# Performance work log

Hardware: AMD Instinct MI355X
Metric: run time of the kernel (lower is better)

The kernel has to match this reference:

```python
import math
import jax, jax.numpy as jnp
import numpy as np

B, L, D = 2, 2048, 512
S, P = 4, 16  # n_orthogonal_sets, planes_per_set
TP = S * P


def setup_inputs() -> dict:
    key = jax.random.key(0)
    ks = jax.random.split(key, 12)
    sc = 0.02
    return {
        "x": jax.random.normal(ks[0], (B, L, D), dtype=jnp.float32),
        "set_weights": jnp.ones((S,), dtype=jnp.float32),
        "kw1": jax.random.normal(ks[1], (D, D), dtype=jnp.float32) * sc,
        "kb1": jnp.zeros((D,), dtype=jnp.float32),
        "kw2": jax.random.normal(ks[2], (D, TP), dtype=jnp.float32) * sc,
        "kb2": jnp.zeros((TP,), dtype=jnp.float32),
        "qw1": jax.random.normal(ks[3], (D, D), dtype=jnp.float32) * sc,
        "qb1": jnp.zeros((D,), dtype=jnp.float32),
        "qw2": jax.random.normal(ks[4], (D, TP), dtype=jnp.float32) * sc,
        "qb2": jnp.zeros((TP,), dtype=jnp.float32),
        "vw": jax.random.normal(ks[5], (D, D), dtype=jnp.float32) * sc,
        "vb": jnp.zeros((D,), dtype=jnp.float32),
        "ln_g": jnp.ones((D,), dtype=jnp.float32),
        "ln_b": jnp.zeros((D,), dtype=jnp.float32),
        "ow": jax.random.normal(ks[6], (D, D), dtype=jnp.float32) * sc,
        "ob": jnp.zeros((D,), dtype=jnp.float32),
    }


def reference(x, set_weights, kw1, kb1, kw2, kb2, qw1, qb1, qw2, qb2, vw, vb, ln_g, ln_b, ow, ob):
    b, l, d = x.shape
    # phase encoders: Linear -> GELU(exact) -> Linear, tanh * pi
    kp = jnp.tanh(jax.nn.gelu(x @ kw1 + kb1, approximate=False) @ kw2 + kb2) * math.pi
    qp = jnp.tanh(jax.nn.gelu(x @ qw1 + qb1, approximate=False) @ qw2 + qb2) * math.pi
    kp = kp.reshape(b, l, S, P)
    qp = qp.reshape(b, l, S, P)
    V = x @ vw + vb  # real values; phasor complex handled as (re, im)
    w = jax.nn.softmax(set_weights)
    total = jnp.zeros((b, l, d), dtype=x.dtype)
    for s in range(S):
        kc, ksn = jnp.cos(kp[:, :, s, :]), jnp.sin(kp[:, :, s, :])  # [b,l,P]
        # bound = e^{i kp} * V (V real); memory = cumsum over time
        Mre = jnp.cumsum(kc[..., None] * V[:, :, None, :], axis=1)  # [b,l,P,d]
        Mim = jnp.cumsum(ksn[..., None] * V[:, :, None, :], axis=1)
        # Re(memory * conj(e^{i qp})) summed over planes
        r = (jnp.einsum('blpd,blp->bld', Mre, jnp.cos(qp[:, :, s, :]))
             + jnp.einsum('blpd,blp->bld', Mim, jnp.sin(qp[:, :, s, :])))
        total = total + w[s] * r
    positions = jnp.arange(1, l + 1, dtype=x.dtype)
    norm = jnp.sqrt(positions * P)[None, :, None]
    y = total / norm
    mu = jnp.mean(y, axis=-1, keepdims=True)
    var = jnp.mean((y - mu) ** 2, axis=-1, keepdims=True)
    yn = (y - mu) / jnp.sqrt(var + 1e-5) * ln_g + ln_b
    return x + yn @ ow + ob
```

## Files before the change

### kernel.cpp

```cpp
#include <hip/hip_runtime.h>
#include <math.h>

constexpr int NB = 2;
constexpr int LQ = 2048;
constexpr int DD = 512;
constexpr int PPL = 16;
constexpr int TPP = 64;
constexpr int FF = 128;
constexpr int NC = 32;
constexpr int TC = 64;
constexpr float PI_F = 3.14159265358979323846f;

typedef __attribute__((ext_vector_type(4))) float f32x4;
typedef __attribute__((ext_vector_type(8))) short bf16x8;

static __device__ __forceinline__ unsigned short f2bf(float x) {
    union { float f; unsigned u; } v; v.f = x;
    unsigned r = v.u + 0x7fff + ((v.u >> 16) & 1);
    return (unsigned short)(r >> 16);
}
static __device__ __forceinline__ float bf2f(unsigned short u) {
    union { unsigned u; float f; } v; v.u = ((unsigned)u) << 16;
    return v.f;
}

__global__ __launch_bounds__(256) void prep_kernel(
    const float* __restrict__ kw1, const float* __restrict__ qw1,
    const float* __restrict__ vw, const float* __restrict__ ow,
    const float* __restrict__ kw2, const float* __restrict__ qw2,
    unsigned short* __restrict__ kw1t, unsigned short* __restrict__ qw1t,
    unsigned short* __restrict__ vwt, unsigned short* __restrict__ owt,
    unsigned short* __restrict__ kw2t, unsigned short* __restrict__ qw2t)
{
    __shared__ float t[32][33];
    const int id = blockIdx.x;
    const int tid = threadIdx.x;
    const float* W;
    unsigned short* O;
    int K, N, n0, k0;
    if (id < 1024) {
        const int mat = id >> 8, rem = id & 255;
        W = (mat == 0) ? kw1 : (mat == 1) ? qw1 : (mat == 2) ? vw : ow;
        O = (mat == 0) ? kw1t : (mat == 1) ? qw1t : (mat == 2) ? vwt : owt;
        K = DD; N = DD;
        n0 = (rem & 15) * 32; k0 = (rem >> 4) * 32;
    } else {
        const int rid = id - 1024;
        const int mat = rid >> 5, rem = rid & 31;
        W = mat ? qw2 : kw2;
        O = mat ? qw2t : kw2t;
        K = DD; N = TPP;
        n0 = (rem & 1) * 32; k0 = (rem >> 1) * 32;
    }
    const int tx = tid & 31, ty = tid >> 5;
#pragma unroll
    for (int i = 0; i < 4; ++i)
        t[ty + 8 * i][tx] = W[(size_t)(k0 + ty + 8 * i) * N + n0 + tx];
    __syncthreads();
#pragma unroll
    for (int i = 0; i < 4; ++i)
        O[(size_t)(n0 + ty + 8 * i) * K + k0 + tx] = f2bf(t[tx][ty + 8 * i]);
}

__global__ __launch_bounds__(256) void mgemm_fused(
    const float* __restrict__ X,
    const unsigned short* __restrict__ kw1t, const unsigned short* __restrict__ qw1t,
    const unsigned short* __restrict__ vwt,
    const float* __restrict__ kb1, const float* __restrict__ qb1, const float* __restrict__ vb,
    unsigned short* __restrict__ hkb, unsigned short* __restrict__ hqb,
    unsigned short* __restrict__ Vt)
{
    const int z = blockIdx.z;
    const unsigned short* Bt = (z == 0) ? kw1t : (z == 1) ? qw1t : vwt;
    const float* bias = (z == 0) ? kb1 : (z == 1) ? qb1 : vb;
    unsigned short* obf = (z == 0) ? hkb : (z == 1) ? hqb : Vt;
    const int K = DD, N = DD;

    __shared__ unsigned short As[128 * 72];
    __shared__ unsigned short Bs[128 * 72];
    const int tid = threadIdx.x;
    const int w = tid >> 6, lane = tid & 63, grp = lane >> 4, lid = lane & 15;
    const int wr = w >> 1, wc = w & 1;
    const int row0 = blockIdx.y * 128, col0 = blockIdx.x * 128;
    f32x4 acc[4][4];
#pragma unroll
    for (int m = 0; m < 4; ++m)
#pragma unroll
        for (int n = 0; n < 4; ++n) acc[m][n] = (f32x4)0.f;

    for (int k0 = 0; k0 < K; k0 += 64) {
        float4 a0[4], a1[4];
        bf16x8 vbv[4];
#pragma unroll
        for (int i = 0; i < 4; ++i) {
            const int c = tid + i * 256;
            const float* ap = X + (size_t)(row0 + (c >> 3)) * K + k0 + (c & 7) * 8;
            a0[i] = *(const float4*)ap;
            a1[i] = *(const float4*)(ap + 4);
            vbv[i] = *(const bf16x8*)(Bt + (size_t)(col0 + (c >> 3)) * K + k0 + (c & 7) * 8);
        }
        __syncthreads();
#pragma unroll
        for (int i = 0; i < 4; ++i) {
            const int c = tid + i * 256;
            ushort4 u0 = {f2bf(a0[i].x), f2bf(a0[i].y), f2bf(a0[i].z), f2bf(a0[i].w)};
            ushort4 u1 = {f2bf(a1[i].x), f2bf(a1[i].y), f2bf(a1[i].z), f2bf(a1[i].w)};
            *(ushort4*)(As + (c >> 3) * 72 + (c & 7) * 8) = u0;
            *(ushort4*)(As + (c >> 3) * 72 + (c & 7) * 8 + 4) = u1;
            *(bf16x8*)(Bs + (c >> 3) * 72 + (c & 7) * 8) = vbv[i];
        }
        __syncthreads();
#pragma unroll
        for (int kk = 0; kk < 2; ++kk) {
            bf16x8 af[4], bfr[4];
#pragma unroll
            for (int m = 0; m < 4; ++m)
                af[m] = *(const bf16x8*)(As + (wr * 64 + m * 16 + lid) * 72 + kk * 32 + grp * 8);
#pragma unroll
            for (int n = 0; n < 4; ++n)
                bfr[n] = *(const bf16x8*)(Bs + (wc * 64 + n * 16 + lid) * 72 + kk * 32 + grp * 8);
#pragma unroll
            for (int m = 0; m < 4; ++m)
#pragma unroll
                for (int n = 0; n < 4; ++n)
                    acc[m][n] = __builtin_amdgcn_mfma_f32_16x16x32_bf16(af[m], bfr[n], acc[m][n], 0, 0, 0);
        }
    }
#pragma unroll
    for (int m = 0; m < 4; ++m) {
#pragma unroll
        for (int n = 0; n < 4; ++n) {
            const int col = col0 + wc * 64 + n * 16 + lid;
            const float bc = bias[col];
            if (z == 2) {
                const int rowb = row0 + wr * 64 + m * 16 + grp * 4;
                const int b = rowb >> 11, l = rowb & (LQ - 1);
                const int c = l >> 6, t0 = l & 63;
                ushort4 u;
                u.x = f2bf(acc[m][n][0] + bc);
                u.y = f2bf(acc[m][n][1] + bc);
                u.z = f2bf(acc[m][n][2] + bc);
                u.w = f2bf(acc[m][n][3] + bc);
                *(ushort4*)(Vt + ((size_t)((b * NC + c) * DD) + col) * TC + t0) = u;
            } else {
#pragma unroll
                for (int r = 0; r < 4; ++r) {
                    const int row = row0 + wr * 64 + m * 16 + grp * 4 + r;
                    float v = acc[m][n][r] + bc;
                    v = 0.5f * v * (1.0f + erff(v * 0.70710678118654752f));
                    obf[(size_t)row * N + col] = f2bf(v);
                }
            }
        }
    }
}

__global__ __launch_bounds__(256) void phase_fused(
    const unsigned short* __restrict__ hkb, const unsigned short* __restrict__ hqb,
    const unsigned short* __restrict__ kw2t, const unsigned short* __restrict__ qw2t,
    const float* __restrict__ kb2, const float* __restrict__ qb2,
    const float* __restrict__ sw,
    unsigned short* __restrict__ CKb, unsigned short* __restrict__ CQb,
    unsigned short* __restrict__ CKt)
{
    const int isq = blockIdx.y;
    const unsigned short* A = isq ? hqb : hkb;
    const unsigned short* Bt = isq ? qw2t : kw2t;
    const float* b2 = isq ? qb2 : kb2;
    unsigned short* FROW = isq ? CQb : CKb;
    const int K = DD;

    __shared__ unsigned short As[64 * 72];
    __shared__ unsigned short Bs[64 * 72];
    const int tid = threadIdx.x;
    const int w = tid >> 6, lane = tid & 63, grp = lane >> 4, lid = lane & 15;
    const int row0 = blockIdx.x * 64;
    f32x4 acc[4];
#pragma unroll
    for (int n = 0; n < 4; ++n) acc[n] = (f32x4)0.f;

    for (int k0 = 0; k0 < K; k0 += 64) {
        bf16x8 va[2], vbv[2];
#pragma unroll
        for (int i = 0; i < 2; ++i) {
            const int c = tid + i * 256;
            va[i] = *(const bf16x8*)(A + (size_t)(row0 + (c >> 3)) * K + k0 + (c & 7) * 8);
            vbv[i] = *(const bf16x8*)(Bt + (size_t)(c >> 3) * K + k0 + (c & 7) * 8);
        }
        __syncthreads();
#pragma unroll
        for (int i = 0; i < 2; ++i) {
            const int c = tid + i * 256;
            *(bf16x8*)(As + (c >> 3) * 72 + (c & 7) * 8) = va[i];
            *(bf16x8*)(Bs + (c >> 3) * 72 + (c & 7) * 8) = vbv[i];
        }
        __syncthreads();
#pragma unroll
        for (int kk = 0; kk < 2; ++kk) {
            bf16x8 af, bfr[4];
            af = *(const bf16x8*)(As + (w * 16 + lid) * 72 + kk * 32 + grp * 8);
#pragma unroll
            for (int n = 0; n < 4; ++n)
                bfr[n] = *(const bf16x8*)(Bs + (n * 16 + lid) * 72 + kk * 32 + grp * 8);
#pragma unroll
            for (int n = 0; n < 4; ++n)
                acc[n] = __builtin_amdgcn_mfma_f32_16x16x32_bf16(af, bfr[n], acc[n], 0, 0, 0);
        }
    }
    float wsm[4] = {1.f, 1.f, 1.f, 1.f};
    if (isq) {
        float s0 = sw[0], s1 = sw[1], s2 = sw[2], s3 = sw[3];
        float mx = fmaxf(fmaxf(s0, s1), fmaxf(s2, s3));
        float e0 = __expf(s0 - mx), e1 = __expf(s1 - mx), e2 = __expf(s2 - mx), e3 = __expf(s3 - mx);
        float inv = 1.0f / (e0 + e1 + e2 + e3);
        wsm[0] = e0 * inv; wsm[1] = e1 * inv; wsm[2] = e2 * inv; wsm[3] = e3 * inv;
    }
#pragma unroll
    for (int n = 0; n < 4; ++n) {
        const int p = n * 16 + lid;
        const float bc = b2[p];
        const float wg = isq ? wsm[p >> 4] : 1.0f;
#pragma unroll
        for (int r = 0; r < 4; ++r) {
            const int row = row0 + w * 16 + grp * 4 + r;
            float u = acc[n][r] + bc;
            float th = 1.0f - 2.0f / (__expf(2.0f * u) + 1.0f);
            float ph = th * PI_F;
            float sp, cp;
            __sincosf(ph, &sp, &cp);
            const unsigned short cb = f2bf(cp * wg), sb = f2bf(sp * wg);
            FROW[(size_t)row * FF + 2 * p + 0] = cb;
            FROW[(size_t)row * FF + 2 * p + 1] = sb;
            if (!isq) {
                const int b = row >> 11, l = row & (LQ - 1);
                const int c = l >> 6, t = l & 63;
                const size_t base = ((size_t)(b * NC + c) * FF) * TC;
                CKt[base + (size_t)(2 * p + 0) * TC + t] = cb;
                CKt[base + (size_t)(2 * p + 1) * TC + t] = sb;
            }
        }
    }
}

__global__ __launch_bounds__(256) void passA_mfma(
    const unsigned short* __restrict__ Vt, const unsigned short* __restrict__ CKt,
    unsigned short* __restrict__ Stp)
{
    const int tid = threadIdx.x;
    const int w = tid >> 6, lane = tid & 63, grp = lane >> 4, lid = lane & 15;
    const int dq = blockIdx.x, c = blockIdx.y, b = blockIdx.z;
    const int d0 = dq * 128 + w * 32;
    const size_t cb = (size_t)(b * NC + c);
    f32x4 acc[2][8];
#pragma unroll
    for (int md = 0; md < 2; ++md)
#pragma unroll
        for (int nf = 0; nf < 8; ++nf) acc[md][nf] = (f32x4)0.f;
#pragma unroll
    for (int kt = 0; kt < 2; ++kt) {
        bf16x8 av[2], bk[8];
#pragma unroll
        for (int md = 0; md < 2; ++md)
            av[md] = *(const bf16x8*)(Vt + (cb * DD + d0 + md * 16 + lid) * TC + kt * 32 + grp * 8);
#pragma unroll
        for (int nf = 0; nf < 8; ++nf)
            bk[nf] = *(const bf16x8*)(CKt + (cb * FF + nf * 16 + lid) * TC + kt * 32 + grp * 8);
#pragma unroll
        for (int md = 0; md < 2; ++md)
#pragma unroll
            for (int nf = 0; nf < 8; ++nf)
                acc[md][nf] = __builtin_amdgcn_mfma_f32_16x16x32_bf16(av[md], bk[nf], acc[md][nf], 0, 0, 0);
    }
#pragma unroll
    for (int md = 0; md < 2; ++md)
#pragma unroll
        for (int nf = 0; nf < 8; ++nf)
#pragma unroll
            for (int r = 0; r < 4; ++r) {
                const int d = d0 + md * 16 + grp * 4 + r;
                const int f = nf * 16 + lid;
                Stp[(cb * DD + d) * FF + f] = f2bf(acc[md][nf][r]);
            }
}

__global__ __launch_bounds__(256) void prefix_mfma(
    const unsigned short* __restrict__ Stp, unsigned short* __restrict__ Stb)
{
    const int gid = blockIdx.x * 256 + threadIdx.x;
    const int b = gid >> 16;
    const int df = gid & 65535;
    float run = 0.f;
#pragma unroll
    for (int c = 0; c < NC; ++c) {
        const size_t idx = ((size_t)(b * NC + c) << 16) + df;
        Stb[idx] = f2bf(run);
        run += bf2f(Stp[idx]);
    }
}

__global__ __launch_bounds__(256) void passC_mfma(
    const unsigned short* __restrict__ CQb, const unsigned short* __restrict__ CKb,
    const unsigned short* __restrict__ Vt, const unsigned short* __restrict__ Stb,
    float* __restrict__ R)
{
    __shared__ unsigned short P[64][72];
    const int tid = threadIdx.x;
    const int w = tid >> 6, lane = tid & 63, grp = lane >> 4, lid = lane & 15;
    const int dh = blockIdx.x, c = blockIdx.y, b = blockIdx.z;
    const size_t rowbase = (size_t)b * LQ + c * 64;
    const size_t cb = (size_t)(b * NC + c);
    f32x4 qk[4];
#pragma unroll
    for (int nt = 0; nt < 4; ++nt) qk[nt] = (f32x4)0.f;
#pragma unroll
    for (int kf = 0; kf < 4; ++kf) {
        bf16x8 aq = *(const bf16x8*)(CQb + (rowbase + w * 16 + lid) * FF + kf * 32 + grp * 8);
        bf16x8 bk[4];
#pragma unroll
        for (int nt = 0; nt < 4; ++nt)
            bk[nt] = *(const bf16x8*)(CKb + (rowbase + nt * 16 + lid) * FF + kf * 32 + grp * 8);
#pragma unroll
        for (int nt = 0; nt < 4; ++nt)
            qk[nt] = __builtin_amdgcn_mfma_f32_16x16x32_bf16(aq, bk[nt], qk[nt], 0, 0, 0);
    }
#pragma unroll
    for (int nt = 0; nt < 4; ++nt)
#pragma unroll
        for (int r = 0; r < 4; ++r) {
            const int row = w * 16 + grp * 4 + r;
            const int col = nt * 16 + lid;
            P[row][col] = f2bf(col <= row ? qk[nt][r] : 0.f);
        }
    __syncthreads();
    const int d0 = dh * 128 + w * 32;
    f32x4 racc[4][2];
#pragma unroll
    for (int ml = 0; ml < 4; ++ml)
#pragma unroll
        for (int nd = 0; nd < 2; ++nd) racc[ml][nd] = (f32x4)0.f;
#pragma unroll
    for (int kt = 0; kt < 2; ++kt) {
        bf16x8 ap[4], bv[2];
#pragma unroll
        for (int ml = 0; ml < 4; ++ml)
            ap[ml] = *(const bf16x8*)&P[ml * 16 + lid][kt * 32 + grp * 8];
#pragma unroll
        for (int nd = 0; nd < 2; ++nd)
            bv[nd] = *(const bf16x8*)(Vt + (cb * DD + d0 + nd * 16 + lid) * TC + kt * 32 + grp * 8);
#pragma unroll
        for (int ml = 0; ml < 4; ++ml)
#pragma unroll
            for (int nd = 0; nd < 2; ++nd)
                racc[ml][nd] = __builtin_amdgcn_mfma_f32_16x16x32_bf16(ap[ml], bv[nd], racc[ml][nd], 0, 0, 0);
    }
#pragma unroll
    for (int kf = 0; kf < 4; ++kf) {
        bf16x8 aq[4], bs[2];
#pragma unroll
        for (int ml = 0; ml < 4; ++ml)
            aq[ml] = *(const bf16x8*)(CQb + (rowbase + ml * 16 + lid) * FF + kf * 32 + grp * 8);
#pragma unroll
        for (int nd = 0; nd < 2; ++nd)
            bs[nd] = *(const bf16x8*)(Stb + (cb * DD + d0 + nd * 16 + lid) * FF + kf * 32 + grp * 8);
#pragma unroll
        for (int ml = 0; ml < 4; ++ml)
#pragma unroll
            for (int nd = 0; nd < 2; ++nd)
                racc[ml][nd] = __builtin_amdgcn_mfma_f32_16x16x32_bf16(aq[ml], bs[nd], racc[ml][nd], 0, 0, 0);
    }
#pragma unroll
    for (int ml = 0; ml < 4; ++ml)
#pragma unroll
        for (int nd = 0; nd < 2; ++nd)
#pragma unroll
            for (int r = 0; r < 4; ++r) {
                const int l = ml * 16 + grp * 4 + r;
                const int d = d0 + nd * 16 + lid;
                R[(rowbase + l) * DD + d] = racc[ml][nd][r];
            }
}

__global__ __launch_bounds__(256) void ln_kernel(
    const float* __restrict__ R, const float* __restrict__ g,
    const float* __restrict__ be, unsigned short* __restrict__ YN)
{
    const int row = blockIdx.x;
    const int l = row & (LQ - 1);
    const int tid = threadIdx.x;
    const float pscale = rsqrtf((float)((l + 1) * PPL));
    float y0 = R[(size_t)row * DD + tid] * pscale;
    float y1 = R[(size_t)row * DD + 256 + tid] * pscale;
    float s = y0 + y1;
    float q = y0 * y0 + y1 * y1;
#pragma unroll
    for (int off = 32; off >= 1; off >>= 1) {
        s += __shfl_xor(s, off, 64);
        q += __shfl_xor(q, off, 64);
    }
    __shared__ float rs[4], rq[4];
    const int wid = tid >> 6, lane = tid & 63;
    if (lane == 0) { rs[wid] = s; rq[wid] = q; }
    __syncthreads();
    const float ts = rs[0] + rs[1] + rs[2] + rs[3];
    const float tq = rq[0] + rq[1] + rq[2] + rq[3];
    const float mu = ts * (1.0f / DD);
    float var = tq * (1.0f / DD) - mu * mu;
    const float rstd = rsqrtf(var + 1e-5f);
    YN[(size_t)row * DD + tid] = f2bf((y0 - mu) * rstd * g[tid] + be[tid]);
    YN[(size_t)row * DD + 256 + tid] = f2bf((y1 - mu) * rstd * g[tid + 256] + be[tid + 256]);
}

__global__ __launch_bounds__(256) void mgemm_out(
    const unsigned short* __restrict__ A, const unsigned short* __restrict__ Bt,
    const float* __restrict__ bias, const float* __restrict__ resid,
    float* __restrict__ out)
{
    const int K = DD, N = DD;
    __shared__ unsigned short As[128 * 72];
    __shared__ unsigned short Bs[64 * 72];
    const int tid = threadIdx.x;
    const int w = tid >> 6, lane = tid & 63, grp = lane >> 4, lid = lane & 15;
    const int wr = w >> 1, wc = w & 1;
    const int row0 = blockIdx.y * 128, col0 = blockIdx.x * 64;
    f32x4 acc[4][2];
#pragma unroll
    for (int m = 0; m < 4; ++m)
#pragma unroll
        for (int n = 0; n < 2; ++n) acc[m][n] = (f32x4)0.f;

    for (int k0 = 0; k0 < K; k0 += 64) {
        bf16x8 va[4], vbv[2];
#pragma unroll
        for (int i = 0; i < 4; ++i) {
            const int c = tid + i * 256;
            va[i] = *(const bf16x8*)(A + (size_t)(row0 + (c >> 3)) * K + k0 + (c & 7) * 8);
        }
#pragma unroll
        for (int i = 0; i < 2; ++i) {
            const int c = tid + i * 256;
            vbv[i] = *(const bf16x8*)(Bt + (size_t)(col0 + (c >> 3)) * K + k0 + (c & 7) * 8);
        }
        __syncthreads();
#pragma unroll
        for (int i = 0; i < 4; ++i) {
            const int c = tid + i * 256;
            *(bf16x8*)(As + (c >> 3) * 72 + (c & 7) * 8) = va[i];
        }
#pragma unroll
        for (int i = 0; i < 2; ++i) {
            const int c = tid + i * 256;
            *(bf16x8*)(Bs + (c >> 3) * 72 + (c & 7) * 8) = vbv[i];
        }
        __syncthreads();
#pragma unroll
        for (int kk = 0; kk < 2; ++kk) {
            bf16x8 af[4], bfr[2];
#pragma unroll
            for (int m = 0; m < 4; ++m)
                af[m] = *(const bf16x8*)(As + (wr * 64 + m * 16 + lid) * 72 + kk * 32 + grp * 8);
#pragma unroll
            for (int n = 0; n < 2; ++n)
                bfr[n] = *(const bf16x8*)(Bs + (wc * 32 + n * 16 + lid) * 72 + kk * 32 + grp * 8);
#pragma unroll
            for (int m = 0; m < 4; ++m)
#pragma unroll
                for (int n = 0; n < 2; ++n)
                    acc[m][n] = __builtin_amdgcn_mfma_f32_16x16x32_bf16(af[m], bfr[n], acc[m][n], 0, 0, 0);
        }
    }
#pragma unroll
    for (int m = 0; m < 4; ++m) {
#pragma unroll
        for (int n = 0; n < 2; ++n) {
            const int col = col0 + wc * 32 + n * 16 + lid;
            const float bc = bias[col];
#pragma unroll
            for (int r = 0; r < 4; ++r) {
                const int row = row0 + wr * 64 + m * 16 + grp * 4 + r;
                out[(size_t)row * N + col] = acc[m][n][r] + bc + resid[(size_t)row * N + col];
            }
        }
    }
}

extern "C" void kernel_launch(void* const* d_in, const int* in_sizes, int n_in,
                              void* d_out, int out_size, void* d_ws, size_t ws_size,
                              hipStream_t stream)
{
    const float* x   = (const float*)d_in[0];
    const float* sw  = (const float*)d_in[1];
    const float* kw1 = (const float*)d_in[2];
    const float* kb1 = (const float*)d_in[3];
    const float* kw2 = (const float*)d_in[4];
    const float* kb2 = (const float*)d_in[5];
    const float* qw1 = (const float*)d_in[6];
    const float* qb1 = (const float*)d_in[7];
    const float* qw2 = (const float*)d_in[8];
    const float* qb2 = (const float*)d_in[9];
    const float* vw  = (const float*)d_in[10];
    const float* vb  = (const float*)d_in[11];
    const float* lng = (const float*)d_in[12];
    const float* lnb = (const float*)d_in[13];
    const float* ow  = (const float*)d_in[14];
    const float* ob  = (const float*)d_in[15];
    float* out = (float*)d_out;

    const size_t MR = (size_t)NB * LQ;
    float* ws = (float*)d_ws;
    float* Rb = ws;
    unsigned short* hkb  = (unsigned short*)(Rb + MR * DD);
    unsigned short* hqb  = hkb + MR * DD;
    unsigned short* YNb  = hqb + MR * DD;
    unsigned short* Vt   = YNb + MR * DD;
    unsigned short* CQb  = Vt + MR * DD;
    unsigned short* CKb  = CQb + MR * FF;
    unsigned short* CKt  = CKb + MR * FF;
    unsigned short* Stp  = CKt + MR * FF;
    unsigned short* Stb  = Stp + (size_t)NB * NC * DD * FF;
    unsigned short* kw1t = Stb + (size_t)NB * NC * DD * FF;
    unsigned short* qw1t = kw1t + (size_t)DD * DD;
    unsigned short* vwt  = qw1t + (size_t)DD * DD;
    unsigned short* owt  = vwt + (size_t)DD * DD;
    unsigned short* kw2t = owt + (size_t)DD * DD;
    unsigned short* qw2t = kw2t + (size_t)TPP * DD;

    const dim3 blk(256);
    hipLaunchKernelGGL(prep_kernel, dim3(1088), blk, 0, stream,
                       kw1, qw1, vw, ow, kw2, qw2,
                       kw1t, qw1t, vwt, owt, kw2t, qw2t);
    hipLaunchKernelGGL(mgemm_fused, dim3(DD / 128, MR / 128, 3), blk, 0, stream,
                       x, kw1t, qw1t, vwt, kb1, qb1, vb, hkb, hqb, Vt);
    hipLaunchKernelGGL(phase_fused, dim3(MR / 64, 2), blk, 0, stream,
                       hkb, hqb, kw2t, qw2t, kb2, qb2, sw, CKb, CQb, CKt);
    hipLaunchKernelGGL(passA_mfma, dim3(4, NC, NB), blk, 0, stream, Vt, CKt, Stp);
    hipLaunchKernelGGL(prefix_mfma, dim3((NB * DD * FF) / 256), blk, 0, stream, Stp, Stb);
    hipLaunchKernelGGL(passC_mfma, dim3(4, NC, NB), blk, 0, stream, CQb, CKb, Vt, Stb, Rb);
    hipLaunchKernelGGL(ln_kernel, dim3((unsigned)MR), blk, 0, stream, Rb, lng, lnb, YNb);
    hipLaunchKernelGGL(mgemm_out, dim3(DD / 64, MR / 128), blk, 0, stream, YNb, owt, ob, x, out);
}
```

Measured before the change: 157.5 us.

## Merge all stages into one persistent cooperative kernel with grid syncs

```diff
diff --git a/kernel.cpp b/kernel.cpp
--- a/kernel.cpp
+++ b/kernel.cpp
@@ -1,5 +1,8 @@
 #include <hip/hip_runtime.h>
+#include <hip/hip_cooperative_groups.h>
 #include <math.h>
+
+namespace cg = cooperative_groups;
 
 constexpr int NB = 2;
 constexpr int LQ = 2048;
@@ -9,6 +12,7 @@
 constexpr int FF = 128;
 constexpr int NC = 32;
 constexpr int TC = 64;
+constexpr int NCU = 256;
 constexpr float PI_F = 3.14159265358979323846f;
 
 typedef __attribute__((ext_vector_type(4))) float f32x4;
@@ -24,460 +28,463 @@
     return v.f;
 }
 
-__global__ __launch_bounds__(256) void prep_kernel(
-    const float* __restrict__ kw1, const float* __restrict__ qw1,
-    const float* __restrict__ vw, const float* __restrict__ ow,
-    const float* __restrict__ kw2, const float* __restrict__ qw2,
-    unsigned short* __restrict__ kw1t, unsigned short* __restrict__ qw1t,
-    unsigned short* __restrict__ vwt, unsigned short* __restrict__ owt,
-    unsigned short* __restrict__ kw2t, unsigned short* __restrict__ qw2t)
+__global__ __launch_bounds__(256, 2) void mega_kernel(
+    const float* __restrict__ x, const float* __restrict__ sw,
+    const float* __restrict__ kw1, const float* __restrict__ kb1,
+    const float* __restrict__ kw2, const float* __restrict__ kb2,
+    const float* __restrict__ qw1, const float* __restrict__ qb1,
+    const float* __restrict__ qw2, const float* __restrict__ qb2,
+    const float* __restrict__ vw, const float* __restrict__ vb,
+    const float* __restrict__ lng, const float* __restrict__ lnb,
+    const float* __restrict__ ow, const float* __restrict__ ob,
+    float* __restrict__ out, void* wsbase)
 {
-    __shared__ float t[32][33];
-    const int id = blockIdx.x;
+    cg::grid_group grid = cg::this_grid();
+    __shared__ unsigned short smem[(128 + 64) * 72];
     const int tid = threadIdx.x;
-    const float* W;
-    unsigned short* O;
-    int K, N, n0, k0;
-    if (id < 1024) {
-        const int mat = id >> 8, rem = id & 255;
-        W = (mat == 0) ? kw1 : (mat == 1) ? qw1 : (mat == 2) ? vw : ow;
-        O = (mat == 0) ? kw1t : (mat == 1) ? qw1t : (mat == 2) ? vwt : owt;
-        K = DD; N = DD;
-        n0 = (rem & 15) * 32; k0 = (rem >> 4) * 32;
-    } else {
-        const int rid = id - 1024;
-        const int mat = rid >> 5, rem = rid & 31;
-        W = mat ? qw2 : kw2;
-        O = mat ? qw2t : kw2t;
-        K = DD; N = TPP;
-        n0 = (rem & 1) * 32; k0 = (rem >> 1) * 32;
-    }
-    const int tx = tid & 31, ty = tid >> 5;
-#pragma unroll
-    for (int i = 0; i < 4; ++i)
-        t[ty + 8 * i][tx] = W[(size_t)(k0 + ty + 8 * i) * N + n0 + tx];
-    __syncthreads();
-#pragma unroll
-    for (int i = 0; i < 4; ++i)
-        O[(size_t)(n0 + ty + 8 * i) * K + k0 + tx] = f2bf(t[tx][ty + 8 * i]);
-}
-
-__global__ __launch_bounds__(256) void mgemm_fused(
-    const float* __restrict__ X,
-    const unsigned short* __restrict__ kw1t, const unsigned short* __restrict__ qw1t,
-    const unsigned short* __restrict__ vwt,
-    const float* __restrict__ kb1, const float* __restrict__ qb1, const float* __restrict__ vb,
-    unsigned short* __restrict__ hkb, unsigned short* __restrict__ hqb,
-    unsigned short* __restrict__ Vt)
-{
-    const int z = blockIdx.z;
-    const unsigned short* Bt = (z == 0) ? kw1t : (z == 1) ? qw1t : vwt;
-    const float* bias = (z == 0) ? kb1 : (z == 1) ? qb1 : vb;
-    unsigned short* obf = (z == 0) ? hkb : (z == 1) ? hqb : Vt;
-    const int K = DD, N = DD;
-
-    __shared__ unsigned short As[128 * 72];
-    __shared__ unsigned short Bs[128 * 72];
-    const int tid = threadIdx.x;
+    const int nb = gridDim.x;
+    const size_t MR = (size_t)NB * LQ;
+
+    float* Rb = (float*)wsbase;
+    unsigned short* xb   = (unsigned short*)(Rb + MR * DD);
+    unsigned short* hkb  = xb + MR * DD;
+    unsigned short* hqb  = hkb + MR * DD;
+    unsigned short* YNb  = hqb + MR * DD;
+    unsigned short* Vt   = YNb + MR * DD;
+    unsigned short* CQb  = Vt + MR * DD;
+    unsigned short* CKb  = CQb + MR * FF;
+    unsigned short* CKt  = CKb + MR * FF;
+    unsigned short* Stp  = CKt + MR * FF;
+    unsigned short* Stb  = Stp + (size_t)NB * NC * DD * FF;
+    unsigned short* kw1t = Stb + (size_t)NB * NC * DD * FF;
+    unsigned short* qw1t = kw1t + (size_t)DD * DD;
+    unsigned short* vwt  = qw1t + (size_t)DD * DD;
+    unsigned short* owt  = vwt + (size_t)DD * DD;
+    unsigned short* kw2t = owt + (size_t)DD * DD;
+    unsigned short* qw2t = kw2t + (size_t)TPP * DD;
+
     const int w = tid >> 6, lane = tid & 63, grp = lane >> 4, lid = lane & 15;
-    const int wr = w >> 1, wc = w & 1;
-    const int row0 = blockIdx.y * 128, col0 = blockIdx.x * 128;
-    f32x4 acc[4][4];
-#pragma unroll
-    for (int m = 0; m < 4; ++m)
-#pragma unroll
-        for (int n = 0; n < 4; ++n) acc[m][n] = (f32x4)0.f;
-
-    for (int k0 = 0; k0 < K; k0 += 64) {
-        float4 a0[4], a1[4];
-        bf16x8 vbv[4];
-#pragma unroll
-        for (int i = 0; i < 4; ++i) {
-            const int c = tid + i * 256;
-            const float* ap = X + (size_t)(row0 + (c >> 3)) * K + k0 + (c & 7) * 8;
-            a0[i] = *(const float4*)ap;
-            a1[i] = *(const float4*)(ap + 4);
-            vbv[i] = *(const bf16x8*)(Bt + (size_t)(col0 + (c >> 3)) * K + k0 + (c & 7) * 8);
-        }
+
+    for (int t = blockIdx.x; t < 2112; t += nb) {
+        if (t < 1024) {
+            const int i = t * 2048 + tid * 8;
+            float4 a = *(const float4*)(x + i);
+            float4 b = *(const float4*)(x + i + 4);
+            ushort4 u0 = {f2bf(a.x), f2bf(a.y), f2bf(a.z), f2bf(a.w)};
+            ushort4 u1 = {f2bf(b.x), f2bf(b.y), f2bf(b.z), f2bf(b.w)};
+            *(ushort4*)(xb + i) = u0;
+            *(ushort4*)(xb + i + 4) = u1;
+        } else {
+            float* tf = (float*)smem;
+            const int id = t - 1024;
+            const float* W;
+            unsigned short* O;
+            int K, N, n0, k0;
+            if (id < 1024) {
+                const int mat = id >> 8, rem = id & 255;
+                W = (mat == 0) ? kw1 : (mat == 1) ? qw1 : (mat == 2) ? vw : ow;
+                O = (mat == 0) ? kw1t : (mat == 1) ? qw1t : (mat == 2) ? vwt : owt;
+                K = DD; N = DD;
+                n0 = (rem & 15) * 32; k0 = (rem >> 4) * 32;
+            } else {
+                const int rid = id - 1024;
+                const int mat = rid >> 5, rem = rid & 31;
+                W = mat ? qw2 : kw2;
+                O = mat ? qw2t : kw2t;
+                K = DD; N = TPP;
+                n0 = (rem & 1) * 32; k0 = (rem >> 1) * 32;
+            }
+            const int tx = tid & 31, ty = tid >> 5;
+            __syncthreads();
+#pragma unroll
+            for (int i = 0; i < 4; ++i)
+                tf[(ty + 8 * i) * 33 + tx] = W[(size_t)(k0 + ty + 8 * i) * N + n0 + tx];
+            __syncthreads();
+#pragma unroll
+            for (int i = 0; i < 4; ++i)
+                O[(size_t)(n0 + ty + 8 * i) * K + k0 + tx] = f2bf(tf[tx * 33 + ty + 8 * i]);
+        }
+    }
+    grid.sync();
+
+    for (int t = blockIdx.x; t < 768; t += nb) {
+        const int cx = t & 7, ry = (t >> 3) & 31, z = t >> 8;
+        const unsigned short* Bt = (z == 0) ? kw1t : (z == 1) ? qw1t : vwt;
+        const float* bias = (z == 0) ? kb1 : (z == 1) ? qb1 : vb;
+        unsigned short* obf = (z == 0) ? hkb : hqb;
+        unsigned short* As = smem;
+        unsigned short* Bs = smem + 128 * 72;
+        const int wr = w >> 1, wc = w & 1;
+        const int row0 = ry * 128, col0 = cx * 64;
+        f32x4 acc[4][2];
+#pragma unroll
+        for (int m = 0; m < 4; ++m)
+#pragma unroll
+            for (int n = 0; n < 2; ++n) acc[m][n] = (f32x4)0.f;
+        for (int k0 = 0; k0 < DD; k0 += 64) {
+            bf16x8 va[4], vbv[2];
+#pragma unroll
+            for (int i = 0; i < 4; ++i) {
+                const int c = tid + i * 256;
+                va[i] = *(const bf16x8*)(xb + (size_t)(row0 + (c >> 3)) * DD + k0 + (c & 7) * 8);
+            }
+#pragma unroll
+            for (int i = 0; i < 2; ++i) {
+                const int c = tid + i * 256;
+                vbv[i] = *(const bf16x8*)(Bt + (size_t)(col0 + (c >> 3)) * DD + k0 + (c & 7) * 8);
+            }
+            __syncthreads();
+#pragma unroll
+            for (int i = 0; i < 4; ++i) {
+                const int c = tid + i * 256;
+                *(bf16x8*)(As + (c >> 3) * 72 + (c & 7) * 8) = va[i];
+            }
+#pragma unroll
+            for (int i = 0; i < 2; ++i) {
+                const int c = tid + i * 256;
+                *(bf16x8*)(Bs + (c >> 3) * 72 + (c & 7) * 8) = vbv[i];
+            }
+            __syncthreads();
+#pragma unroll
+            for (int kk = 0; kk < 2; ++kk) {
+                bf16x8 af[4], bfr[2];
+#pragma unroll
+                for (int m = 0; m < 4; ++m)
+                    af[m] = *(const bf16x8*)(As + (wr * 64 + m * 16 + lid) * 72 + kk * 32 + grp * 8);
+#pragma unroll
+                for (int n = 0; n < 2; ++n)
+                    bfr[n] = *(const bf16x8*)(Bs + (wc * 32 + n * 16 + lid) * 72 + kk * 32 + grp * 8);
+#pragma unroll
+                for (int m = 0; m < 4; ++m)
+#pragma unroll
+                    for (int n = 0; n < 2; ++n)
+                        acc[m][n] = __builtin_amdgcn_mfma_f32_16x16x32_bf16(af[m], bfr[n], acc[m][n], 0, 0, 0);
+            }
+        }
+#pragma unroll
+        for (int m = 0; m < 4; ++m) {
+#pragma unroll
+            for (int n = 0; n < 2; ++n) {
+                const int col = col0 + wc * 32 + n * 16 + lid;
+                const float bc = bias[col];
+                if (z == 2) {
+                    const int rowb = row0 + wr * 64 + m * 16 + grp * 4;
+                    const int b = rowb >> 11, l = rowb & (LQ - 1);
+                    const int c = l >> 6, t0 = l & 63;
+                    ushort4 u;
+                    u.x = f2bf(acc[m][n][0] + bc);
+                    u.y = f2bf(acc[m][n][1] + bc);
+                    u.z = f2bf(acc[m][n][2] + bc);
+                    u.w = f2bf(acc[m][n][3] + bc);
+                    *(ushort4*)(Vt + ((size_t)((b * NC + c) * DD) + col) * TC + t0) = u;
+                } else {
+#pragma unroll
+                    for (int r = 0; r < 4; ++r) {
+                        const int row = row0 + wr * 64 + m * 16 + grp * 4 + r;
+                        float v = acc[m][n][r] + bc;
+                        v = 0.5f * v * (1.0f + erff(v * 0.70710678118654752f));
+                        obf[(size_t)row * DD + col] = f2bf(v);
+                    }
+                }
+            }
+        }
+    }
+    grid.sync();
+
+    for (int t = blockIdx.x; t < 128; t += nb) {
+        const int isq = t >> 6;
+        const int row0 = (t & 63) * 64;
+        const unsigned short* A = isq ? hqb : hkb;
+        const unsigned short* Bt = isq ? qw2t : kw2t;
+        const float* b2 = isq ? qb2 : kb2;
+        unsigned short* FROW = isq ? CQb : CKb;
+        unsigned short* As = smem;
+        unsigned short* Bs = smem + 64 * 72;
+        f32x4 acc[4];
+#pragma unroll
+        for (int n = 0; n < 4; ++n) acc[n] = (f32x4)0.f;
+        for (int k0 = 0; k0 < DD; k0 += 64) {
+            bf16x8 va[2], vbv[2];
+#pragma unroll
+            for (int i = 0; i < 2; ++i) {
+                const int c = tid + i * 256;
+                va[i] = *(const bf16x8*)(A + (size_t)(row0 + (c >> 3)) * DD + k0 + (c & 7) * 8);
+                vbv[i] = *(const bf16x8*)(Bt + (size_t)(c >> 3) * DD + k0 + (c & 7) * 8);
+            }
+            __syncthreads();
+#pragma unroll
+            for (int i = 0; i < 2; ++i) {
+                const int c = tid + i * 256;
+                *(bf16x8*)(As + (c >> 3) * 72 + (c & 7) * 8) = va[i];
+                *(bf16x8*)(Bs + (c >> 3) * 72 + (c & 7) * 8) = vbv[i];
+            }
+            __syncthreads();
+#pragma unroll
+            for (int kk = 0; kk < 2; ++kk) {
+                bf16x8 af = *(const bf16x8*)(As + (w * 16 + lid) * 72 + kk * 32 + grp * 8);
+                bf16x8 bfr[4];
+#pragma unroll
+                for (int n = 0; n < 4; ++n)
+                    bfr[n] = *(const bf16x8*)(Bs + (n * 16 + lid) * 72 + kk * 32 + grp * 8);
+#pragma unroll
+                for (int n = 0; n < 4; ++n)
+                    acc[n] = __builtin_amdgcn_mfma_f32_16x16x32_bf16(af, bfr[n], acc[n], 0, 0, 0);
+            }
+        }
+        float wsm[4] = {1.f, 1.f, 1.f, 1.f};
+        if (isq) {
+            float s0 = sw[0], s1 = sw[1], s2 = sw[2], s3 = sw[3];
+            float mx = fmaxf(fmaxf(s0, s1), fmaxf(s2, s3));
+            float e0 = __expf(s0 - mx), e1 = __expf(s1 - mx), e2 = __expf(s2 - mx), e3 = __expf(s3 - mx);
+            float inv = 1.0f / (e0 + e1 + e2 + e3);
+            wsm[0] = e0 * inv; wsm[1] = e1 * inv; wsm[2] = e2 * inv; wsm[3] = e3 * inv;
+        }
+#pragma unroll
+        for (int n = 0; n < 4; ++n) {
+            const int p = n * 16 + lid;
+            const float bc = b2[p];
+            const float wg = isq ? wsm[p >> 4] : 1.0f;
+#pragma unroll
+            for (int r = 0; r < 4; ++r) {
+                const int row = row0 + w * 16 + grp * 4 + r;
+                float u = acc[n][r] + bc;
+                float th = 1.0f - 2.0f / (__expf(2.0f * u) + 1.0f);
+                float ph = th * PI_F;
+                float sp, cp;
+                __sincosf(ph, &sp, &cp);
+                const unsigned short cb = f2bf(cp * wg), sb = f2bf(sp * wg);
+                FROW[(size_t)row * FF + 2 * p + 0] = cb;
+                FROW[(size_t)row * FF + 2 * p + 1] = sb;
+                if (!isq) {
+                    const int b = row >> 11, l = row & (LQ - 1);
+                    const int c = l >> 6, tt = l & 63;
+                    const size_t base = ((size_t)(b * NC + c) * FF) * TC;
+                    CKt[base + (size_t)(2 * p + 0) * TC + tt] = cb;
+                    CKt[base + (size_t)(2 * p + 1) * TC + tt] = sb;
+                }
+            }
+        }
+    }
+    grid.sync();
+
+    for (int t = blockIdx.x; t < 512; t += nb) {
+        const int dq = t & 7, c = (t >> 3) & 31, b = t >> 8;
+        const size_t cb = (size_t)(b * NC + c);
+        const int d0 = dq * 64 + (w >> 1) * 32;
+        const int f0 = (w & 1) * 64;
+        f32x4 acc[2][4];
+#pragma unroll
+        for (int md = 0; md < 2; ++md)
+#pragma unroll
+            for (int nf = 0; nf < 4; ++nf) acc[md][nf] = (f32x4)0.f;
+#pragma unroll
+        for (int kt = 0; kt < 2; ++kt) {
+            bf16x8 av[2], bk[4];
+#pragma unroll
+            for (int md = 0; md < 2; ++md)
+                av[md] = *(const bf16x8*)(Vt + (cb * DD + d0 + md * 16 + lid) * TC + kt * 32 + grp * 8);
+#pragma unroll
+            for (int nf = 0; nf < 4; ++nf)
+                bk[nf] = *(const bf16x8*)(CKt + (cb * FF + f0 + nf * 16 + lid) * TC + kt * 32 + grp * 8);
+#pragma unroll
+            for (int md = 0; md < 2; ++md)
+#pragma unroll
+                for (int nf = 0; nf < 4; ++nf)
+                    acc[md][nf] = __builtin_amdgcn_mfma_f32_16x16x32_bf16(av[md], bk[nf], acc[md][nf], 0, 0, 0);
+        }
+#pragma unroll
+        for (int md = 0; md < 2; ++md)
+#pragma unroll
+            for (int nf = 0; nf < 4; ++nf)
+#pragma unroll
+                for (int r = 0; r < 4; ++r) {
+                    const int d = d0 + md * 16 + grp * 4 + r;
+                    const int f = f0 + nf * 16 + lid;
+                    Stp[(cb * DD + d) * FF + f] = f2bf(acc[md][nf][r]);
+                }
+    }
+    grid.sync();
+
+    for (int gid = blockIdx.x * 256 + tid; gid < NB * DD * FF; gid += nb * 256) {
+        const int df = gid & 65535;
+        const int b = gid >> 16;
+        float run = 0.f;
+#pragma unroll
+        for (int c = 0; c < NC; ++c) {
+            const size_t idx = ((size_t)(b * NC + c) << 16) + df;
+            Stb[idx] = f2bf(run);
+            run += bf2f(Stp[idx]);
+        }
+    }
+    grid.sync();
+
+    for (int t = blockIdx.x; t < 256; t += nb) {
+        const int dh = t & 3, c = (t >> 2) & 31, b = t >> 7;
+        const size_t rowbase = (size_t)b * LQ + c * 64;
+        const size_t cb = (size_t)(b * NC + c);
+        unsigned short (*P)[72] = (unsigned short(*)[72])smem;
         __syncthreads();
-#pragma unroll
-        for (int i = 0; i < 4; ++i) {
-            const int c = tid + i * 256;
-            ushort4 u0 = {f2bf(a0[i].x), f2bf(a0[i].y), f2bf(a0[i].z), f2bf(a0[i].w)};
-            ushort4 u1 = {f2bf(a1[i].x), f2bf(a1[i].y), f2bf(a1[i].z), f2bf(a1[i].w)};
-            *(ushort4*)(As + (c >> 3) * 72 + (c & 7) * 8) = u0;
-            *(ushort4*)(As + (c >> 3) * 72 + (c & 7) * 8 + 4) = u1;
-            *(bf16x8*)(Bs + (c >> 3) * 72 + (c & 7) * 8) = vbv[i];
-        }
+        f32x4 qk[4];
+#pragma unroll
+        for (int nt = 0; nt < 4; ++nt) qk[nt] = (f32x4)0.f;
+#pragma unroll
+        for (int kf = 0; kf < 4; ++kf) {
+            bf16x8 aq = *(const bf16x8*)(CQb + (rowbase + w * 16 + lid) * FF + kf * 32 + grp * 8);
+            bf16x8 bk[4];
+#pragma unroll
+            for (int nt = 0; nt < 4; ++nt)
+                bk[nt] = *(const bf16x8*)(CKb + (rowbase + nt * 16 + lid) * FF + kf * 32 + grp * 8);
+#pragma unroll
+            for (int nt = 0; nt < 4; ++nt)
+                qk[nt] = __builtin_amdgcn_mfma_f32_16x16x32_bf16(aq, bk[nt], qk[nt], 0, 0, 0);
+        }
+#pragma unroll
+        for (int nt = 0; nt < 4; ++nt)
+#pragma unroll
+            for (int r = 0; r < 4; ++r) {
+                const int row = w * 16 + grp * 4 + r;
+                const int col = nt * 16 + lid;
+                P[row][col] = f2bf(col <= row ? qk[nt][r] : 0.f);
+            }
         __syncthreads();
-#pragma unroll
-        for (int kk = 0; kk < 2; ++kk) {
-            bf16x8 af[4], bfr[4];
-#pragma unroll
-            for (int m = 0; m < 4; ++m)
-                af[m] = *(const bf16x8*)(As + (wr * 64 + m * 16 + lid) * 72 + kk * 32 + grp * 8);
-#pragma unroll
-            for (int n = 0; n < 4; ++n)
-                bfr[n] = *(const bf16x8*)(Bs + (wc * 64 + n * 16 + lid) * 72 + kk * 32 + grp * 8);
-#pragma unroll
-            for (int m = 0; m < 4; ++m)
-#pragma unroll
-                for (int n = 0; n < 4; ++n)
-                    acc[m][n] = __builtin_amdgcn_mfma_f32_16x16x32_bf16(af[m], bfr[n], acc[m][n], 0, 0, 0);
-        }
-    }
-#pragma unroll
-    for (int m = 0; m < 4; ++m) {
-#pragma unroll
-        for (int n = 0; n < 4; ++n) {
-            const int col = col0 + wc * 64 + n * 16 + lid;
-            const float bc = bias[col];
-            if (z == 2) {
-                const int rowb = row0 + wr * 64 + m * 16 + grp * 4;
-                const int b = rowb >> 11, l = rowb & (LQ - 1);
-                const int c = l >> 6, t0 = l & 63;
-                ushort4 u;
-                u.x = f2bf(acc[m][n][0] + bc);
-                u.y = f2bf(acc[m][n][1] + bc);
-                u.z = f2bf(acc[m][n][2] + bc);
-                u.w = f2bf(acc[m][n][3] + bc);
-                *(ushort4*)(Vt + ((size_t)((b * NC + c) * DD) + col) * TC + t0) = u;
-            } else {
+        const int d0 = dh * 128 + w * 32;
+        f32x4 racc[4][2];
+#pragma unroll
+        for (int ml = 0; ml < 4; ++ml)
+#pragma unroll
+            for (int nd = 0; nd < 2; ++nd) racc[ml][nd] = (f32x4)0.f;
+#pragma unroll
+        for (int kt = 0; kt < 2; ++kt) {
+            bf16x8 ap[4], bv[2];
+#pragma unroll
+            for (int ml = 0; ml < 4; ++ml)
+                ap[ml] = *(const bf16x8*)&P[ml * 16 + lid][kt * 32 + grp * 8];
+#pragma unroll
+            for (int nd = 0; nd < 2; ++nd)
+                bv[nd] = *(const bf16x8*)(Vt + (cb * DD + d0 + nd * 16 + lid) * TC + kt * 32 + grp * 8);
+#pragma unroll
+            for (int ml = 0; ml < 4; ++ml)
+#pragma unroll
+                for (int nd = 0; nd < 2; ++nd)
+                    racc[ml][nd] = __builtin_amdgcn_mfma_f32_16x16x32_bf16(ap[ml], bv[nd], racc[ml][nd], 0, 0, 0);
+        }
+#pragma unroll
+        for (int kf = 0; kf < 4; ++kf) {
+            bf16x8 aq[4], bs[2];
+#pragma unroll
+            for (int ml = 0; ml < 4; ++ml)
+                aq[ml] = *(const bf16x8*)(CQb + (rowbase + ml * 16 + lid) * FF + kf * 32 + grp * 8);
+#pragma unroll
+            for (int nd = 0; nd < 2; ++nd)
+                bs[nd] = *(const bf16x8*)(Stb + (cb * DD + d0 + nd * 16 + lid) * FF + kf * 32 + grp * 8);
+#pragma unroll
+            for (int ml = 0; ml < 4; ++ml)
+#pragma unroll
+                for (int nd = 0; nd < 2; ++nd)
+                    racc[ml][nd] = __builtin_amdgcn_mfma_f32_16x16x32_bf16(aq[ml], bs[nd], racc[ml][nd], 0, 0, 0);
+        }
+#pragma unroll
+        for (int ml = 0; ml < 4; ++ml)
+#pragma unroll
+            for (int nd = 0; nd < 2; ++nd)
+#pragma unroll
+                for (int r = 0; r < 4; ++r) {
+                    const int l = ml * 16 + grp * 4 + r;
+                    const int d = d0 + nd * 16 + lid;
+                    Rb[(rowbase + l) * DD + d] = racc[ml][nd][r];
+                }
+    }
+    grid.sync();
+
+    for (int row = blockIdx.x; row < (int)MR; row += nb) {
+        float* sred = (float*)smem;
+        __syncthreads();
+        const int l = row & (LQ - 1);
+        const float pscale = rsqrtf((float)((l + 1) * PPL));
+        float y0 = Rb[(size_t)row * DD + tid] * pscale;
+        float y1 = Rb[(size_t)row * DD + 256 + tid] * pscale;
+        float s = y0 + y1;
+        float q = y0 * y0 + y1 * y1;
+#pragma unroll
+        for (int off = 32; off >= 1; off >>= 1) {
+            s += __shfl_xor(s, off, 64);
+            q += __shfl_xor(q, off, 64);
+        }
+        const int wid = tid >> 6;
+        if (lane == 0) { sred[wid] = s; sred[4 + wid] = q; }
+        __syncthreads();
+        const float ts = sred[0] + sred[1] + sred[2] + sred[3];
+        const float tq = sred[4] + sred[5] + sred[6] + sred[7];
+        const float mu = ts * (1.0f / DD);
+        float var = tq * (1.0f / DD) - mu * mu;
+        const float rstd = rsqrtf(var + 1e-5f);
+        YNb[(size_t)row * DD + tid] = f2bf((y0 - mu) * rstd * lng[tid] + lnb[tid]);
+        YNb[(size_t)row * DD + 256 + tid] = f2bf((y1 - mu) * rstd * lng[tid + 256] + lnb[tid + 256]);
+    }
+    grid.sync();
+
+    for (int t = blockIdx.x; t < 256; t += nb) {
+        const int cx = t & 7, ry = t >> 3;
+        unsigned short* As = smem;
+        unsigned short* Bs = smem + 128 * 72;
+        const int wr = w >> 1, wc = w & 1;
+        const int row0 = ry * 128, col0 = cx * 64;
+        f32x4 acc[4][2];
+#pragma unroll
+        for (int m = 0; m < 4; ++m)
+#pragma unroll
+            for (int n = 0; n < 2; ++n) acc[m][n] = (f32x4)0.f;
+        for (int k0 = 0; k0 < DD; k0 += 64) {
+            bf16x8 va[4], vbv[2];
+#pragma unroll
+            for (int i = 0; i < 4; ++i) {
+                const int c = tid + i * 256;
+                va[i] = *(const bf16x8*)(YNb + (size_t)(row0 + (c >> 3)) * DD + k0 + (c & 7) * 8);
+            }
+#pragma unroll
+            for (int i = 0; i < 2; ++i) {
+                const int c = tid + i * 256;
+                vbv[i] = *(const bf16x8*)(owt + (size_t)(col0 + (c >> 3)) * DD + k0 + (c & 7) * 8);
+            }
+            __syncthreads();
+#pragma unroll
+            for (int i = 0; i < 4; ++i) {
+                const int c = tid + i * 256;
+                *(bf16x8*)(As + (c >> 3) * 72 + (c & 7) * 8) = va[i];
+            }
+#pragma unroll
+            for (int i = 0; i < 2; ++i) {
+                const int c = tid + i * 256;
+                *(bf16x8*)(Bs + (c >> 3) * 72 + (c & 7) * 8) = vbv[i];
+            }
+            __syncthreads();
+#pragma unroll
+            for (int kk = 0; kk < 2; ++kk) {
+                bf16x8 af[4], bfr[2];
+#pragma unroll
+                for (int m = 0; m < 4; ++m)
+                    af[m] = *(const bf16x8*)(As + (wr * 64 + m * 16 + lid) * 72 + kk * 32 + grp * 8);
+#pragma unroll
+                for (int n = 0; n < 2; ++n)
+                    bfr[n] = *(const bf16x8*)(Bs + (wc * 32 + n * 16 + lid) * 72 + kk * 32 + grp * 8);
+#pragma unroll
+                for (int m = 0; m < 4; ++m)
+#pragma unroll
+                    for (int n = 0; n < 2; ++n)
+                        acc[m][n] = __builtin_amdgcn_mfma_f32_16x16x32_bf16(af[m], bfr[n], acc[m][n], 0, 0, 0);
+            }
+        }
+#pragma unroll
+        for (int m = 0; m < 4; ++m) {
+#pragma unroll
+            for (int n = 0; n < 2; ++n) {
+                const int col = col0 + wc * 32 + n * 16 + lid;
+                const float bc = ob[col];
 #pragma unroll
                 for (int r = 0; r < 4; ++r) {
                     const int row = row0 + wr * 64 + m * 16 + grp * 4 + r;
-                    float v = acc[m][n][r] + bc;
-                    v = 0.5f * v * (1.0f + erff(v * 0.70710678118654752f));
-                    obf[(size_t)row * N + col] = f2bf(v);
+                    out[(size_t)row * DD + col] = acc[m][n][r] + bc + x[(size_t)row * DD + col];
                 }
-            }
-        }
-    }
-}
-
-__global__ __launch_bounds__(256) void phase_fused(
-    const unsigned short* __restrict__ hkb, const unsigned short* __restrict__ hqb,
-    const unsigned short* __restrict__ kw2t, const unsigned short* __restrict__ qw2t,
-    const float* __restrict__ kb2, const float* __restrict__ qb2,
-    const float* __restrict__ sw,
-    unsigned short* __restrict__ CKb, unsigned short* __restrict__ CQb,
-    unsigned short* __restrict__ CKt)
-{
-    const int isq = blockIdx.y;
-    const unsigned short* A = isq ? hqb : hkb;
-    const unsigned short* Bt = isq ? qw2t : kw2t;
-    const float* b2 = isq ? qb2 : kb2;
-    unsigned short* FROW = isq ? CQb : CKb;
-    const int K = DD;
-
-    __shared__ unsigned short As[64 * 72];
-    __shared__ unsigned short Bs[64 * 72];
-    const int tid = threadIdx.x;
-    const int w = tid >> 6, lane = tid & 63, grp = lane >> 4, lid = lane & 15;
-    const int row0 = blockIdx.x * 64;
-    f32x4 acc[4];
-#pragma unroll
-    for (int n = 0; n < 4; ++n) acc[n] = (f32x4)0.f;
-
-    for (int k0 = 0; k0 < K; k0 += 64) {
-        bf16x8 va[2], vbv[2];
-#pragma unroll
-        for (int i = 0; i < 2; ++i) {
-            const int c = tid + i * 256;
-            va[i] = *(const bf16x8*)(A + (size_t)(row0 + (c >> 3)) * K + k0 + (c & 7) * 8);
-            vbv[i] = *(const bf16x8*)(Bt + (size_t)(c >> 3) * K + k0 + (c & 7) * 8);
-        }
-        __syncthreads();
-#pragma unroll
-        for (int i = 0; i < 2; ++i) {
-            const int c = tid + i * 256;
-            *(bf16x8*)(As + (c >> 3) * 72 + (c & 7) * 8) = va[i];
-            *(bf16x8*)(Bs + (c >> 3) * 72 + (c & 7) * 8) = vbv[i];
-        }
-        __syncthreads();
-#pragma unroll
-        for (int kk = 0; kk < 2; ++kk) {
-            bf16x8 af, bfr[4];
-            af = *(const bf16x8*)(As + (w * 16 + lid) * 72 + kk * 32 + grp * 8);
-#pragma unroll
-            for (int n = 0; n < 4; ++n)
-                bfr[n] = *(const bf16x8*)(Bs + (n * 16 + lid) * 72 + kk * 32 + grp * 8);
-#pragma unroll
-            for (int n = 0; n < 4; ++n)
-                acc[n] = __builtin_amdgcn_mfma_f32_16x16x32_bf16(af, bfr[n], acc[n], 0, 0, 0);
-        }
-    }
-    float wsm[4] = {1.f, 1.f, 1.f, 1.f};
-    if (isq) {
-        float s0 = sw[0], s1 = sw[1], s2 = sw[2], s3 = sw[3];
-        float mx = fmaxf(fmaxf(s0, s1), fmaxf(s2, s3));
-        float e0 = __expf(s0 - mx), e1 = __expf(s1 - mx), e2 = __expf(s2 - mx), e3 = __expf(s3 - mx);
-        float inv = 1.0f / (e0 + e1 + e2 + e3);
-        wsm[0] = e0 * inv; wsm[1] = e1 * inv; wsm[2] = e2 * inv; wsm[3] = e3 * inv;
-    }
-#pragma unroll
-    for (int n = 0; n < 4; ++n) {
-        const int p = n * 16 + lid;
-        const float bc = b2[p];
-        const float wg = isq ? wsm[p >> 4] : 1.0f;
-#pragma unroll
-        for (int r = 0; r < 4; ++r) {
-            const int row = row0 + w * 16 + grp * 4 + r;
-            float u = acc[n][r] + bc;
-            float th = 1.0f - 2.0f / (__expf(2.0f * u) + 1.0f);
-            float ph = th * PI_F;
-            float sp, cp;
-            __sincosf(ph, &sp, &cp);
-            const unsigned short cb = f2bf(cp * wg), sb = f2bf(sp * wg);
-            FROW[(size_t)row * FF + 2 * p + 0] = cb;
-            FROW[(size_t)row * FF + 2 * p + 1] = sb;
-            if (!isq) {
-                const int b = row >> 11, l = row & (LQ - 1);
-                const int c = l >> 6, t = l & 63;
-                const size_t base = ((size_t)(b * NC + c) * FF) * TC;
-                CKt[base + (size_t)(2 * p + 0) * TC + t] = cb;
-                CKt[base + (size_t)(2 * p + 1) * TC + t] = sb;
-            }
-        }
-    }
-}
-
-__global__ __launch_bounds__(256) void passA_mfma(
-    const unsigned short* __restrict__ Vt, const unsigned short* __restrict__ CKt,
-    unsigned short* __restrict__ Stp)
-{
-    const int tid = threadIdx.x;
-    const int w = tid >> 6, lane = tid & 63, grp = lane >> 4, lid = lane & 15;
-    const int dq = blockIdx.x, c = blockIdx.y, b = blockIdx.z;
-    const int d0 = dq * 128 + w * 32;
-    const size_t cb = (size_t)(b * NC + c);
-    f32x4 acc[2][8];
-#pragma unroll
-    for (int md = 0; md < 2; ++md)
-#pragma unroll
-        for (int nf = 0; nf < 8; ++nf) acc[md][nf] = (f32x4)0.f;
-#pragma unroll
-    for (int kt = 0; kt < 2; ++kt) {
-        bf16x8 av[2], bk[8];
-#pragma unroll
-        for (int md = 0; md < 2; ++md)
-            av[md] = *(const bf16x8*)(Vt + (cb * DD + d0 + md * 16 + lid) * TC + kt * 32 + grp * 8);
-#pragma unroll
-        for (int nf = 0; nf < 8; ++nf)
-            bk[nf] = *(const bf16x8*)(CKt + (cb * FF + nf * 16 + lid) * TC + kt * 32 + grp * 8);
-#pragma unroll
-        for (int md = 0; md < 2; ++md)
-#pragma unroll
-            for (int nf = 0; nf < 8; ++nf)
-                acc[md][nf] = __builtin_amdgcn_mfma_f32_16x16x32_bf16(av[md], bk[nf], acc[md][nf], 0, 0, 0);
-    }
-#pragma unroll
-    for (int md = 0; md < 2; ++md)
-#pragma unroll
-        for (int nf = 0; nf < 8; ++nf)
-#pragma unroll
-            for (int r = 0; r < 4; ++r) {
-                const int d = d0 + md * 16 + grp * 4 + r;
-                const int f = nf * 16 + lid;
-                Stp[(cb * DD + d) * FF + f] = f2bf(acc[md][nf][r]);
-            }
-}
-
-__global__ __launch_bounds__(256) void prefix_mfma(
-    const unsigned short* __restrict__ Stp, unsigned short* __restrict__ Stb)
-{
-    const int gid = blockIdx.x * 256 + threadIdx.x;
-    const int b = gid >> 16;
-    const int df = gid & 65535;
-    float run = 0.f;
-#pragma unroll
-    for (int c = 0; c < NC; ++c) {
-        const size_t idx = ((size_t)(b * NC + c) << 16) + df;
-        Stb[idx] = f2bf(run);
-        run += bf2f(Stp[idx]);
-    }
-}
-
-__global__ __launch_bounds__(256) void passC_mfma(
-    const unsigned short* __restrict__ CQb, const unsigned short* __restrict__ CKb,
-    const unsigned short* __restrict__ Vt, const unsigned short* __restrict__ Stb,
-    float* __restrict__ R)
-{
-    __shared__ unsigned short P[64][72];
-    const int tid = threadIdx.x;
-    const int w = tid >> 6, lane = tid & 63, grp = lane >> 4, lid = lane & 15;
-    const int dh = blockIdx.x, c = blockIdx.y, b = blockIdx.z;
-    const size_t rowbase = (size_t)b * LQ + c * 64;
-    const size_t cb = (size_t)(b * NC + c);
-    f32x4 qk[4];
-#pragma unroll
-    for (int nt = 0; nt < 4; ++nt) qk[nt] = (f32x4)0.f;
-#pragma unroll
-    for (int kf = 0; kf < 4; ++kf) {
-        bf16x8 aq = *(const bf16x8*)(CQb + (rowbase + w * 16 + lid) * FF + kf * 32 + grp * 8);
-        bf16x8 bk[4];
-#pragma unroll
-        for (int nt = 0; nt < 4; ++nt)
-            bk[nt] = *(const bf16x8*)(CKb + (rowbase + nt * 16 + lid) * FF + kf * 32 + grp * 8);
-#pragma unroll
-        for (int nt = 0; nt < 4; ++nt)
-            qk[nt] = __builtin_amdgcn_mfma_f32_16x16x32_bf16(aq, bk[nt], qk[nt], 0, 0, 0);
-    }
-#pragma unroll
-    for (int nt = 0; nt < 4; ++nt)
-#pragma unroll
-        for (int r = 0; r < 4; ++r) {
-            const int row = w * 16 + grp * 4 + r;
-            const int col = nt * 16 + lid;
-            P[row][col] = f2bf(col <= row ? qk[nt][r] : 0.f);
-        }
-    __syncthreads();
-    const int d0 = dh * 128 + w * 32;
-    f32x4 racc[4][2];
-#pragma unroll
-    for (int ml = 0; ml < 4; ++ml)
-#pragma unroll
-        for (int nd = 0; nd < 2; ++nd) racc[ml][nd] = (f32x4)0.f;
-#pragma unroll
-    for (int kt = 0; kt < 2; ++kt) {
-        bf16x8 ap[4], bv[2];
-#pragma unroll
-        for (int ml = 0; ml < 4; ++ml)
-            ap[ml] = *(const bf16x8*)&P[ml * 16 + lid][kt * 32 + grp * 8];
-#pragma unroll
-        for (int nd = 0; nd < 2; ++nd)
-            bv[nd] = *(const bf16x8*)(Vt + (cb * DD + d0 + nd * 16 + lid) * TC + kt * 32 + grp * 8);
-#pragma unroll
-        for (int ml = 0; ml < 4; ++ml)
-#pragma unroll
-            for (int nd = 0; nd < 2; ++nd)
-                racc[ml][nd] = __builtin_amdgcn_mfma_f32_16x16x32_bf16(ap[ml], bv[nd], racc[ml][nd], 0, 0, 0);
-    }
-#pragma unroll
-    for (int kf = 0; kf < 4; ++kf) {
-        bf16x8 aq[4], bs[2];
-#pragma unroll
-        for (int ml = 0; ml < 4; ++ml)
-            aq[ml] = *(const bf16x8*)(CQb + (rowbase + ml * 16 + lid) * FF + kf * 32 + grp * 8);
-#pragma unroll
-        for (int nd = 0; nd < 2; ++nd)
-            bs[nd] = *(const bf16x8*)(Stb + (cb * DD + d0 + nd * 16 + lid) * FF + kf * 32 + grp * 8);
-#pragma unroll
-        for (int ml = 0; ml < 4; ++ml)
-#pragma unroll
-            for (int nd = 0; nd < 2; ++nd)
-                racc[ml][nd] = __builtin_amdgcn_mfma_f32_16x16x32_bf16(aq[ml], bs[nd], racc[ml][nd], 0, 0, 0);
-    }
-#pragma unroll
-    for (int ml = 0; ml < 4; ++ml)
-#pragma unroll
-        for (int nd = 0; nd < 2; ++nd)
-#pragma unroll
-            for (int r = 0; r < 4; ++r) {
-                const int l = ml * 16 + grp * 4 + r;
-                const int d = d0 + nd * 16 + lid;
-                R[(rowbase + l) * DD + d] = racc[ml][nd][r];
-            }
-}
-
-__global__ __launch_bounds__(256) void ln_kernel(
-    const float* __restrict__ R, const float* __restrict__ g,
-    const float* __restrict__ be, unsigned short* __restrict__ YN)
-{
-    const int row = blockIdx.x;
-    const int l = row & (LQ - 1);
-    const int tid = threadIdx.x;
-    const float pscale = rsqrtf((float)((l + 1) * PPL));
-    float y0 = R[(size_t)row * DD + tid] * pscale;
-    float y1 = R[(size_t)row * DD + 256 + tid] * pscale;
-    float s = y0 + y1;
-    float q = y0 * y0 + y1 * y1;
-#pragma unroll
-    for (int off = 32; off >= 1; off >>= 1) {
-        s += __shfl_xor(s, off, 64);
-        q += __shfl_xor(q, off, 64);
-    }
-    __shared__ float rs[4], rq[4];
-    const int wid = tid >> 6, lane = tid & 63;
-    if (lane == 0) { rs[wid] = s; rq[wid] = q; }
-    __syncthreads();
-    const float ts = rs[0] + rs[1] + rs[2] + rs[3];
-    const float tq = rq[0] + rq[1] + rq[2] + rq[3];
-    const float mu = ts * (1.0f / DD);
-    float var = tq * (1.0f / DD) - mu * mu;
-    const float rstd = rsqrtf(var + 1e-5f);
-    YN[(size_t)row * DD + tid] = f2bf((y0 - mu) * rstd * g[tid] + be[tid]);
-    YN[(size_t)row * DD + 256 + tid] = f2bf((y1 - mu) * rstd * g[tid + 256] + be[tid + 256]);
-}
-
-__global__ __launch_bounds__(256) void mgemm_out(
-    const unsigned short* __restrict__ A, const unsigned short* __restrict__ Bt,
-    const float* __restrict__ bias, const float* __restrict__ resid,
-    float* __restrict__ out)
-{
-    const int K = DD, N = DD;
-    __shared__ unsigned short As[128 * 72];
-    __shared__ unsigned short Bs[64 * 72];
-    const int tid = threadIdx.x;
-    const int w = tid >> 6, lane = tid & 63, grp = lane >> 4, lid = lane & 15;
-    const int wr = w >> 1, wc = w & 1;
-    const int row0 = blockIdx.y * 128, col0 = blockIdx.x * 64;
-    f32x4 acc[4][2];
-#pragma unroll
-    for (int m = 0; m < 4; ++m)
-#pragma unroll
-        for (int n = 0; n < 2; ++n) acc[m][n] = (f32x4)0.f;
-
-    for (int k0 = 0; k0 < K; k0 += 64) {
-        bf16x8 va[4], vbv[2];
-#pragma unroll
-        for (int i = 0; i < 4; ++i) {
-            const int c = tid + i * 256;
-            va[i] = *(const bf16x8*)(A + (size_t)(row0 + (c >> 3)) * K + k0 + (c & 7) * 8);
-        }
-#pragma unroll
-        for (int i = 0; i < 2; ++i) {
-            const int c = tid + i * 256;
-            vbv[i] = *(const bf16x8*)(Bt + (size_t)(col0 + (c >> 3)) * K + k0 + (c & 7) * 8);
-        }
-        __syncthreads();
-#pragma unroll
-        for (int i = 0; i < 4; ++i) {
-            const int c = tid + i * 256;
-            *(bf16x8*)(As + (c >> 3) * 72 + (c & 7) * 8) = va[i];
-        }
-#pragma unroll
-        for (int i = 0; i < 2; ++i) {
-            const int c = tid + i * 256;
-            *(bf16x8*)(Bs + (c >> 3) * 72 + (c & 7) * 8) = vbv[i];
-        }
-        __syncthreads();
-#pragma unroll
-        for (int kk = 0; kk < 2; ++kk) {
-            bf16x8 af[4], bfr[2];
-#pragma unroll
-            for (int m = 0; m < 4; ++m)
-                af[m] = *(const bf16x8*)(As + (wr * 64 + m * 16 + lid) * 72 + kk * 32 + grp * 8);
-#pragma unroll
-            for (int n = 0; n < 2; ++n)
-                bfr[n] = *(const bf16x8*)(Bs + (wc * 32 + n * 16 + lid) * 72 + kk * 32 + grp * 8);
-#pragma unroll
-            for (int m = 0; m < 4; ++m)
-#pragma unroll
-                for (int n = 0; n < 2; ++n)
-                    acc[m][n] = __builtin_amdgcn_mfma_f32_16x16x32_bf16(af[m], bfr[n], acc[m][n], 0, 0, 0);
-        }
-    }
-#pragma unroll
-    for (int m = 0; m < 4; ++m) {
-#pragma unroll
-        for (int n = 0; n < 2; ++n) {
-            const int col = col0 + wc * 32 + n * 16 + lid;
-            const float bc = bias[col];
-#pragma unroll
-            for (int r = 0; r < 4; ++r) {
-                const int row = row0 + wr * 64 + m * 16 + grp * 4 + r;
-                out[(size_t)row * N + col] = acc[m][n][r] + bc + resid[(size_t)row * N + col];
             }
         }
     }
@@ -503,38 +510,24 @@
     const float* lnb = (const float*)d_in[13];
     const float* ow  = (const float*)d_in[14];
     const float* ob  = (const float*)d_in[15];
-    float* out = (float*)d_out;
-
-    const size_t MR = (size_t)NB * LQ;
-    float* ws = (float*)d_ws;
-    float* Rb = ws;
-    unsigned short* hkb  = (unsigned short*)(Rb + MR * DD);
-    unsigned short* hqb  = hkb + MR * DD;
-    unsigned short* YNb  = hqb + MR * DD;
-    unsigned short* Vt   = YNb + MR * DD;
-    unsigned short* CQb  = Vt + MR * DD;
-    unsigned short* CKb  = CQb + MR * FF;
-    unsigned short* CKt  = CKb + MR * FF;
-    unsigned short* Stp  = CKt + MR * FF;
-    unsigned short* Stb  = Stp + (size_t)NB * NC * DD * FF;
-    unsigned short* kw1t = Stb + (size_t)NB * NC * DD * FF;
-    unsigned short* qw1t = kw1t + (size_t)DD * DD;
-    unsigned short* vwt  = qw1t + (size_t)DD * DD;
-    unsigned short* owt  = vwt + (size_t)DD * DD;
-    unsigned short* kw2t = owt + (size_t)DD * DD;
-    unsigned short* qw2t = kw2t + (size_t)TPP * DD;
-
-    const dim3 blk(256);
-    hipLaunchKernelGGL(prep_kernel, dim3(1088), blk, 0, stream,
-                       kw1, qw1, vw, ow, kw2, qw2,
-                       kw1t, qw1t, vwt, owt, kw2t, qw2t);
-    hipLaunchKernelGGL(mgemm_fused, dim3(DD / 128, MR / 128, 3), blk, 0, stream,
-                       x, kw1t, qw1t, vwt, kb1, qb1, vb, hkb, hqb, Vt);
-    hipLaunchKernelGGL(phase_fused, dim3(MR / 64, 2), blk, 0, stream,
-                       hkb, hqb, kw2t, qw2t, kb2, qb2, sw, CKb, CQb, CKt);
-    hipLaunchKernelGGL(passA_mfma, dim3(4, NC, NB), blk, 0, stream, Vt, CKt, Stp);
-    hipLaunchKernelGGL(prefix_mfma, dim3((NB * DD * FF) / 256), blk, 0, stream, Stp, Stb);
-    hipLaunchKernelGGL(passC_mfma, dim3(4, NC, NB), blk, 0, stream, CQb, CKb, Vt, Stb, Rb);
-    hipLaunchKernelGGL(ln_kernel, dim3((unsigned)MR), blk, 0, stream, Rb, lng, lnb, YNb);
-    hipLaunchKernelGGL(mgemm_out, dim3(DD / 64, MR / 128), blk, 0, stream, YNb, owt, ob, x, out);
+    float* outp = (float*)d_out;
+    void* wsv = d_ws;
+
+    int occ = 0;
+    hipError_t qe = hipOccupancyMaxActiveBlocksPerMultiprocessor(&occ, mega_kernel, 256, 0);
+    if (qe != hipSuccess || occ < 1) occ = 1;
+    int grid = occ * NCU;
+    if (grid > 512) grid = 512;
+
+    void* args[] = {
+        (void*)&x, (void*)&sw, (void*)&kw1, (void*)&kb1, (void*)&kw2, (void*)&kb2,
+        (void*)&qw1, (void*)&qb1, (void*)&qw2, (void*)&qb2, (void*)&vw, (void*)&vb,
+        (void*)&lng, (void*)&lnb, (void*)&ow, (void*)&ob, (void*)&outp, (void*)&wsv
+    };
+    hipError_t le = hipLaunchCooperativeKernel((const void*)mega_kernel, dim3(grid), dim3(256),
+                                               args, 0, stream);
+    if (le != hipSuccess && grid != NCU) {
+        hipLaunchCooperativeKernel((const void*)mega_kernel, dim3(NCU), dim3(256),
+                                   args, 0, stream);
+    }
 }
```

Result: slower. 410.4 us (+160.6%).
